# Kernel optimization log

Measured on AMD Instinct MI355X. Metric: run time of the kernel, lower is better.

The kernel has to match this reference:

```python
import jax, jax.numpy as jnp
import numpy as np

TEMPERATURE = 0.1
EPS = 1e-07


def setup_inputs() -> dict:
    key = jax.random.key(0)
    k1, k2 = jax.random.split(key)
    embeddings = jax.random.normal(k1, (4096, 768), dtype=jnp.float32)
    labels = jax.random.normal(k2, (4096, 2), dtype=jnp.float32)
    return {"embeddings": embeddings, "labels": labels}


def _supcr_dim(sims, exp_sims, lab, eps):
    # sims, exp_sims: [M, M]; lab: [M]
    M = lab.shape[0]
    dists = jnp.abs(lab[None, :] - lab[:, None])            # [M, M]
    idx = jnp.argsort(dists, axis=1)                         # row-wise sort order
    sorted_d = jnp.take_along_axis(dists, idx, axis=1)
    sorted_s = jnp.take_along_axis(exp_sims, idx, axis=1)
    # reversed cumsum (suffix sums) along each row
    suffix = jnp.flip(jnp.cumsum(jnp.flip(sorted_s, axis=1), axis=1), axis=1)
    # per-row searchsorted: first index where sorted_d >= dists[i, j]
    pos = jax.vmap(lambda sd, rd: jnp.searchsorted(sd, rd, side='left'))(sorted_d, dists)
    denom = jnp.maximum(jnp.take_along_axis(suffix, pos, axis=1), eps)
    # -log(exp(sims) / denom) == log(denom) - sims
    row_loss = jnp.log(denom) - sims
    off_diag = ~jnp.eye(M, dtype=bool)
    total = jnp.sum(jnp.where(off_diag, row_loss, 0.0))
    return total / (M * (M - 1))


def reference(embeddings, labels):
    # cosine similarity / temperature (torch F.normalize clamps norm at 1e-12)
    norm = jnp.maximum(jnp.linalg.norm(embeddings, axis=1, keepdims=True), 1e-12)
    normed = embeddings / norm
    sims = (normed @ normed.T) / TEMPERATURE                 # [M, M]
    exp_sims = jnp.exp(sims)
    # vmap over label dimensions (labels.T: [num_dims, M])
    losses = jax.vmap(lambda lab: _supcr_dim(sims, exp_sims, lab, EPS))(labels.T)
    return losses
```

## Files before the change

### kernel.cpp

```cpp
#include <hip/hip_runtime.h>
#include <hip/hip_bf16.h>
#include <math.h>

#define MM 4096
#define KK 768
#define NB64 64
#define NBK 1024
#define QSCALE 65536.0f
#define LN2 0.6931471805599453f

typedef short bf16x8 __attribute__((ext_vector_type(8)));
typedef unsigned short u16x8 __attribute__((ext_vector_type(8)));
typedef float f32x4 __attribute__((ext_vector_type(4)));

__device__ __forceinline__ float bf2f(unsigned short u) {
  return __uint_as_float(((unsigned int)u) << 16);
}
__device__ __forceinline__ unsigned short f2bf(float f) {
  __hip_bfloat16 h = __float2bfloat16(f);
  return *(unsigned short*)&h;
}

__device__ __forceinline__ void gload16(const void* g, void* l) {
#if __has_builtin(__builtin_amdgcn_global_load_lds)
  __builtin_amdgcn_global_load_lds((__attribute__((address_space(1))) void*)g,
                                   (__attribute__((address_space(3))) void*)l,
                                   16, 0, 0);
#else
  *(bf16x8*)l = *(const bf16x8*)g;
#endif
}

__global__ __launch_bounds__(256) void knorm(const float* __restrict__ emb,
                                             __hip_bfloat16* __restrict__ nb,
                                             const float* __restrict__ labels,
                                             float* __restrict__ dmm) {
  const int tid = threadIdx.x;
  if (blockIdx.x == MM / 4) {
    float mn0 = 1e30f, mx0 = -1e30f, mn1 = 1e30f, mx1 = -1e30f;
    for (int q = tid; q < MM; q += 256) {
      float2 l2 = ((const float2*)labels)[q];
      mn0 = fminf(mn0, l2.x); mx0 = fmaxf(mx0, l2.x);
      mn1 = fminf(mn1, l2.y); mx1 = fmaxf(mx1, l2.y);
    }
    for (int s = 32; s; s >>= 1) {
      mn0 = fminf(mn0, __shfl_down(mn0, s, 64));
      mx0 = fmaxf(mx0, __shfl_down(mx0, s, 64));
      mn1 = fminf(mn1, __shfl_down(mn1, s, 64));
      mx1 = fmaxf(mx1, __shfl_down(mx1, s, 64));
    }
    __shared__ float redm[4][4];
    if ((tid & 63) == 0) {
      redm[0][tid >> 6] = mn0; redm[1][tid >> 6] = mx0;
      redm[2][tid >> 6] = mn1; redm[3][tid >> 6] = mx1;
    }
    __syncthreads();
    if (tid == 0) {
      dmm[0] = fminf(fminf(redm[0][0], redm[0][1]), fminf(redm[0][2], redm[0][3]));
      dmm[1] = fmaxf(fmaxf(redm[1][0], redm[1][1]), fmaxf(redm[1][2], redm[1][3]));
      dmm[2] = fminf(fminf(redm[2][0], redm[2][1]), fminf(redm[2][2], redm[2][3]));
      dmm[3] = fmaxf(fmaxf(redm[3][0], redm[3][1]), fmaxf(redm[3][2], redm[3][3]));
    }
    return;
  }
  const int w = tid >> 6, l = tid & 63;
  const int row = blockIdx.x * 4 + w;
  const float4* e4 = (const float4*)(emb + (size_t)row * KK);
  float4 a = e4[l], b = e4[l + 64], c = e4[l + 128];
  float ss = a.x * a.x + a.y * a.y + a.z * a.z + a.w * a.w +
             b.x * b.x + b.y * b.y + b.z * b.z + b.w * b.w +
             c.x * c.x + c.y * c.y + c.z * c.z + c.w * c.w;
#pragma unroll
  for (int s = 1; s < 64; s <<= 1) ss += __shfl_xor(ss, s, 64);
  const float inv = 1.f / fmaxf(sqrtf(ss), 1e-12f);
  unsigned short* o = (unsigned short*)(nb + (size_t)row * KK);
  ushort4 o1 = {f2bf(a.x * inv), f2bf(a.y * inv), f2bf(a.z * inv), f2bf(a.w * inv)};
  ushort4 o2 = {f2bf(b.x * inv), f2bf(b.y * inv), f2bf(b.z * inv), f2bf(b.w * inv)};
  ushort4 o3 = {f2bf(c.x * inv), f2bf(c.y * inv), f2bf(c.z * inv), f2bf(c.w * inv)};
  *(ushort4*)(o + l * 4) = o1;
  *(ushort4*)(o + 256 + l * 4) = o2;
  *(ushort4*)(o + 512 + l * 4) = o3;
}

union SmemU64 {
  struct { short As[64 * 64]; short Bs[64 * 64]; } s;
  float tbuf[32][68];
};

__global__ __launch_bounds__(256) void kgemm_sym64(const __hip_bfloat16* __restrict__ A,
                                                   unsigned short* __restrict__ out,
                                                   float* __restrict__ srow) {
  __shared__ __align__(16) SmemU64 sm;
  const int tid = threadIdx.x;
  const int w = tid >> 6, l = tid & 63;
  const int wr = w >> 1, wc = w & 1;
  const int b = blockIdx.x;
  int by = (int)((129.0f - sqrtf(16641.0f - 8.0f * (float)b)) * 0.5f);
  by = min(max(by, 0), 63);
  while (by > 0 && (by * (129 - by)) / 2 > b) --by;
  while (by < 63 && (((by + 1) * (129 - (by + 1))) / 2) <= b) ++by;
  const int bx = by + (b - (by * (129 - by)) / 2);
  const int row0 = by * 64, col0 = bx * 64;
  const short* Ag = (const short*)A;

  f32x4 acc[2][2];
#pragma unroll
  for (int mi = 0; mi < 2; ++mi)
#pragma unroll
    for (int ni = 0; ni < 2; ++ni) acc[mi][ni] = (f32x4){0.f, 0.f, 0.f, 0.f};

  const int r0 = tid >> 3, s0 = tid & 7;
  const int sx = ((s0 ^ (r0 & 7)) * 8);
  const int lr = l & 15, kb = (l >> 4) * 8;
  const int xr = (lr & 7) << 3;

  for (int k0 = 0; k0 < KK; k0 += 64) {
    __syncthreads();
    gload16(Ag + (size_t)(row0 + r0) * KK + k0 + sx, &sm.s.As[tid * 8]);
    gload16(Ag + (size_t)(row0 + 32 + r0) * KK + k0 + sx, &sm.s.As[(tid + 256) * 8]);
    gload16(Ag + (size_t)(col0 + r0) * KK + k0 + sx, &sm.s.Bs[tid * 8]);
    gload16(Ag + (size_t)(col0 + 32 + r0) * KK + k0 + sx, &sm.s.Bs[(tid + 256) * 8]);
    __syncthreads();
    bf16x8 av[2][2], bv[2][2];
#pragma unroll
    for (int mi = 0; mi < 2; ++mi)
#pragma unroll
      for (int kh = 0; kh < 2; ++kh)
        av[mi][kh] = *(const bf16x8*)&sm.s.As[(wr * 32 + mi * 16 + lr) * 64 +
                                              ((kh * 32 + kb) ^ xr)];
#pragma unroll
    for (int ni = 0; ni < 2; ++ni)
#pragma unroll
      for (int kh = 0; kh < 2; ++kh)
        bv[ni][kh] = *(const bf16x8*)&sm.s.Bs[(wc * 32 + ni * 16 + lr) * 64 +
                                              ((kh * 32 + kb) ^ xr)];
#pragma unroll
    for (int kh = 0; kh < 2; ++kh)
#pragma unroll
      for (int mi = 0; mi < 2; ++mi)
#pragma unroll
        for (int ni = 0; ni < 2; ++ni)
          acc[mi][ni] = __builtin_amdgcn_mfma_f32_16x16x32_bf16(av[mi][kh], bv[ni][kh],
                                                                acc[mi][ni], 0, 0, 0);
  }

  const int quad = l >> 4;
  const bool diag = (bx == by);

#pragma unroll
  for (int mi = 0; mi < 2; ++mi) {
#pragma unroll
    for (int r = 0; r < 4; ++r) {
      const int grow = row0 + wr * 32 + mi * 16 + quad * 4 + r;
      float rsum = 0.f;
#pragma unroll
      for (int ni = 0; ni < 2; ++ni) {
        const int gcol = col0 + wc * 32 + ni * 16 + lr;
        rsum += (diag && gcol == grow) ? 0.f : acc[mi][ni][r];
      }
#pragma unroll
      for (int mask = 1; mask < 16; mask <<= 1) rsum += __shfl_xor(rsum, mask, 64);
      if (lr == 0) srow[(size_t)grow * 128 + bx * 2 + wc] = rsum / 0.1f;
    }
  }

  if (!diag) {
#pragma unroll
    for (int ni = 0; ni < 2; ++ni) {
      float csum = 0.f;
#pragma unroll
      for (int mi = 0; mi < 2; ++mi)
#pragma unroll
        for (int r = 0; r < 4; ++r) csum += acc[mi][ni][r];
      csum += __shfl_xor(csum, 16, 64);
      csum += __shfl_xor(csum, 32, 64);
      if (quad == 0)
        srow[(size_t)(col0 + wc * 32 + ni * 16 + l) * 128 + by * 2 + wr] = csum / 0.1f;
    }
  }

#pragma unroll
  for (int mi = 0; mi < 2; ++mi)
#pragma unroll
    for (int ni = 0; ni < 2; ++ni)
#pragma unroll
      for (int r = 0; r < 4; ++r)
        acc[mi][ni][r] = __expf(acc[mi][ni][r] / 0.1f);

#pragma unroll
  for (int mi = 0; mi < 2; ++mi)
#pragma unroll
    for (int r = 0; r < 4; ++r) {
      const int grow = row0 + wr * 32 + mi * 16 + quad * 4 + r;
#pragma unroll
      for (int ni = 0; ni < 2; ++ni)
        out[(size_t)grow * MM + col0 + wc * 32 + ni * 16 + lr] = f2bf(acc[mi][ni][r]);
    }

  if (!diag) {
#pragma unroll
    for (int p = 0; p < 2; ++p) {
      __syncthreads();
      if (wc == p) {
#pragma unroll
        for (int ni = 0; ni < 2; ++ni) {
          const int ltr = ni * 16 + lr;
#pragma unroll
          for (int mi = 0; mi < 2; ++mi) {
            const int cbase = wr * 32 + mi * 16 + quad * 4;
#pragma unroll
            for (int r = 0; r < 4; ++r)
              sm.tbuf[ltr][cbase + r] = acc[mi][ni][r];
          }
        }
      }
      __syncthreads();
      const int trow = tid >> 3;
      const int cseg = (tid & 7) * 8;
      const int gtr = col0 + p * 32 + trow;
      u16x8 vv;
#pragma unroll
      for (int q = 0; q < 8; ++q) vv[q] = f2bf(sm.tbuf[trow][cseg + q]);
      *(u16x8*)(out + (size_t)gtr * MM + row0 + cseg) = vv;
    }
  }
}

__global__ __launch_bounds__(256) void kgemm(const __hip_bfloat16* __restrict__ A,
                                             int rowBase,
                                             unsigned short* __restrict__ out,
                                             float* __restrict__ srow) {
  __shared__ __align__(16) short As[128 * 32];
  __shared__ __align__(16) short Bs[128 * 32];
  const int tid = threadIdx.x;
  const int w = tid >> 6, l = tid & 63;
  const int wr = w >> 1, wc = w & 1;
  const int bx = blockIdx.x;
  const int row0 = rowBase + blockIdx.y * 128;
  const int col0 = bx * 128;
  const short* Ag = (const short*)A;

  f32x4 acc[4][4];
#pragma unroll
  for (int mi = 0; mi < 4; ++mi)
#pragma unroll
    for (int ni = 0; ni < 4; ++ni) acc[mi][ni] = (f32x4){0.f, 0.f, 0.f, 0.f};

  const int r0 = tid >> 2, s0 = tid & 3;
  const int r1 = (tid + 256) >> 2;
  const int lrow = l & 15, kb = (l >> 4) * 8;

  for (int k0 = 0; k0 < KK; k0 += 32) {
    __syncthreads();
    gload16(Ag + (size_t)(row0 + r0) * KK + k0 + s0 * 8, &As[tid * 8]);
    gload16(Ag + (size_t)(row0 + r1) * KK + k0 + s0 * 8, &As[(tid + 256) * 8]);
    gload16(Ag + (size_t)(col0 + r0) * KK + k0 + s0 * 8, &Bs[tid * 8]);
    gload16(Ag + (size_t)(col0 + r1) * KK + k0 + s0 * 8, &Bs[(tid + 256) * 8]);
    __syncthreads();
    bf16x8 av[4], bv[4];
#pragma unroll
    for (int mi = 0; mi < 4; ++mi)
      av[mi] = *(const bf16x8*)&As[(wr * 64 + mi * 16 + lrow) * 32 + kb];
#pragma unroll
    for (int ni = 0; ni < 4; ++ni)
      bv[ni] = *(const bf16x8*)&Bs[(wc * 64 + ni * 16 + lrow) * 32 + kb];
#pragma unroll
    for (int mi = 0; mi < 4; ++mi)
#pragma unroll
      for (int ni = 0; ni < 4; ++ni)
        acc[mi][ni] = __builtin_amdgcn_mfma_f32_16x16x32_bf16(av[mi], bv[ni],
                                                              acc[mi][ni], 0, 0, 0);
  }

  const int quad = l >> 4;
#pragma unroll
  for (int mi = 0; mi < 4; ++mi) {
#pragma unroll
    for (int r = 0; r < 4; ++r) {
      const int grow = row0 + wr * 64 + mi * 16 + quad * 4 + r;
      float rsum = 0.f;
#pragma unroll
      for (int ni = 0; ni < 4; ++ni) {
        const int gcol = col0 + wc * 64 + ni * 16 + lrow;
        float a = acc[mi][ni][r];
        out[(size_t)(grow - rowBase) * MM + gcol] = f2bf(__expf(a / 0.1f));
        rsum += (gcol == grow) ? 0.f : a;
      }
#pragma unroll
      for (int mask = 1; mask < 16; mask <<= 1) rsum += __shfl_xor(rsum, mask, 64);
      if (lrow == 0) srow[(size_t)grow * 128 + bx * 2 + wc] = rsum / 0.1f;
    }
  }
}

__global__ __launch_bounds__(256) void kloss(const unsigned short* __restrict__ expb,
                                             int rowBase,
                                             const float* __restrict__ labels,
                                             const float* __restrict__ dmm,
                                             const float* __restrict__ srow,
                                             float* __restrict__ part_logd,
                                             float* __restrict__ part_sr) {
  const int i = rowBase + blockIdx.x;
  const unsigned short* row = expb + (size_t)blockIdx.x * MM;
  __shared__ __align__(16) unsigned long long histU[2 * NBK];
  __shared__ unsigned long long wsumU[4];
  __shared__ float redf[4];
  __shared__ float redsr[4];
  const int tid = threadIdx.x;
  const int lane = tid & 63, wid = tid >> 6;
  const int m0 = tid * 16;
  const int b0 = tid * 8;

  float sv = (tid < 128) ? srow[(size_t)i * 128 + tid] : 0.f;
  for (int s = 32; s; s >>= 1) sv += __shfl_down(sv, s, 64);
  if (lane == 0) redsr[wid] = sv;

  const float c0 = labels[(size_t)i * 2], c1 = labels[(size_t)i * 2 + 1];
  const float tmax0 = fmaxf(fmaxf(c0 - dmm[0], dmm[1] - c0), 1e-30f);
  const float tmax1 = fmaxf(fmaxf(c1 - dmm[2], dmm[3] - c1), 1e-30f);
  const float scale0 = (float)NBK / tmax0;
  const float scale1 = (float)NBK / tmax1;

#pragma unroll
  for (int q = 0; q < 4; ++q)
    ((uint4*)histU)[tid + 256 * q] = (uint4){0, 0, 0, 0};
  __syncthreads();

  {
    u16x8 a = *(const u16x8*)(row + m0);
    u16x8 bq = *(const u16x8*)(row + m0 + 8);
    const float4* lp4 = (const float4*)(labels + (size_t)m0 * 2);
#pragma unroll
    for (int q = 0; q < 8; ++q) {
      float4 v4 = lp4[q];
      const unsigned short r0u = (2 * q < 8) ? a[2 * q] : bq[2 * q - 8];
      const unsigned short r1u = (2 * q + 1 < 8) ? a[2 * q + 1] : bq[2 * q + 1 - 8];
      const unsigned long long g0 =
          (unsigned long long)(unsigned int)(bf2f(r0u) * QSCALE + 0.5f) | (1ULL << 32);
      const unsigned long long g1 =
          (unsigned long long)(unsigned int)(bf2f(r1u) * QSCALE + 0.5f) | (1ULL << 32);
      const int a0 = min((int)(fabsf(v4.x - c0) * scale0), NBK - 1);
      const int a1 = min((int)(fabsf(v4.y - c1) * scale1), NBK - 1);
      const int b2 = min((int)(fabsf(v4.z - c0) * scale0), NBK - 1);
      const int b3 = min((int)(fabsf(v4.w - c1) * scale1), NBK - 1);
      atomicAdd(&histU[a0], g0);
      atomicAdd(&histU[NBK + a1], g0);
      atomicAdd(&histU[b2], g1);
      atomicAdd(&histU[NBK + b3], g1);
    }
  }
  __syncthreads();

  unsigned long long hh[8];
#pragma unroll
  for (int q = 0; q < 4; ++q) {
    uint4 t4 = *(const uint4*)&histU[b0 + 2 * q];
    hh[2 * q] = (unsigned long long)t4.x | ((unsigned long long)t4.y << 32);
    hh[2 * q + 1] = (unsigned long long)t4.z | ((unsigned long long)t4.w << 32);
  }
  unsigned long long S = 0;
#pragma unroll
  for (int u = 0; u < 8; ++u) S += hh[u];
  unsigned long long v = S;
#pragma unroll
  for (int s = 1; s < 64; s <<= 1) {
    unsigned long long t2 = __shfl_down(v, s, 64);
    if (lane + s < 64) v += t2;
  }
  if (lane == 0) wsumU[wid] = v;
  __syncthreads();
  unsigned long long woff = (wid == 0) ? wsumU[1] : ((wid == 2) ? wsumU[3] : 0ULL);
  unsigned long long run = woff + (v - S);

  float acc2 = 0.f;
#pragma unroll
  for (int u = 7; u >= 0; --u) {
    run += hh[u];
    const float nf = (float)(unsigned int)(hh[u] >> 32);
    const float sufq = (float)(unsigned int)run;
    acc2 += nf * __log2f(fmaxf(sufq, 1.f));
  }

  for (int s = 32; s; s >>= 1) acc2 += __shfl_down(acc2, s, 64);
  if (lane == 0) redf[wid] = acc2;
  __syncthreads();
  if (tid == 0) {
    const float tf0 = (float)(unsigned int)(wsumU[0] + wsumU[1]);
    const float tf1 = (float)(unsigned int)(wsumU[2] + wsumU[3]);
    part_logd[i] = (redf[0] + redf[1] - 65536.f - __log2f(tf0) + 16.f) * LN2;
    part_logd[MM + i] = (redf[2] + redf[3] - 65536.f - __log2f(tf1) + 16.f) * LN2;
    part_sr[i] = redsr[0] + redsr[1];
  }
}

__global__ __launch_bounds__(256) void kred1(const float* __restrict__ part_logd,
                                             const float* __restrict__ part_sr,
                                             double* __restrict__ red3) {
  const int tid = threadIdx.x;
  const int base = blockIdx.x * 64;
  double ss = 0.0, s0 = 0.0, s1 = 0.0;
  if (tid < 64) {
    s0 = (double)part_logd[base + tid];
    s1 = (double)part_logd[MM + base + tid];
    ss = (double)part_sr[base + tid];
  }
  for (int s = 32; s; s >>= 1) {
    s0 += __shfl_down(s0, s, 64);
    s1 += __shfl_down(s1, s, 64);
    ss += __shfl_down(ss, s, 64);
  }
  __shared__ double red[3][4];
  if ((tid & 63) == 0) {
    red[0][tid >> 6] = s0; red[1][tid >> 6] = s1; red[2][tid >> 6] = ss;
  }
  __syncthreads();
  if (tid == 0) {
    red3[blockIdx.x * 3 + 0] = red[0][0] + red[0][1] + red[0][2] + red[0][3];
    red3[blockIdx.x * 3 + 1] = red[1][0] + red[1][1] + red[1][2] + red[1][3];
    red3[blockIdx.x * 3 + 2] = red[2][0] + red[2][1] + red[2][2] + red[2][3];
  }
}

__global__ __launch_bounds__(64) void kred2(const double* __restrict__ red3,
                                            float* __restrict__ out) {
  const int t = threadIdx.x;
  double s0 = red3[t * 3 + 0], s1 = red3[t * 3 + 1], ss = red3[t * 3 + 2];
  for (int s = 32; s; s >>= 1) {
    s0 += __shfl_down(s0, s, 64);
    s1 += __shfl_down(s1, s, 64);
    ss += __shfl_down(ss, s, 64);
  }
  if (t == 0) {
    const double n = (double)MM * (double)(MM - 1);
    out[0] = (float)((s0 - ss) / n);
    out[1] = (float)((s1 - ss) / n);
  }
}

extern "C" void kernel_launch(void* const* d_in, const int* in_sizes, int n_in,
                              void* d_out, int out_size, void* d_ws, size_t ws_size,
                              hipStream_t stream) {
  const float* emb = (const float*)d_in[0];
  const float* labels = (const float*)d_in[1];
  float* out = (float*)d_out;
  char* ws = (char*)d_ws;

  size_t off = 0;
  auto alloc = [&](size_t bytes) {
    void* p = ws + off;
    off = (off + bytes + 255) & ~(size_t)255;
    return p;
  };
  __hip_bfloat16* nb = (__hip_bfloat16*)alloc((size_t)MM * KK * 2);
  float* dmm = (float*)alloc(4 * 4);
  float* part_logd = (float*)alloc((size_t)2 * MM * 4);
  float* part_sr = (float*)alloc((size_t)MM * 4);
  float* srow = (float*)alloc((size_t)MM * 128 * 4);
  double* red3 = (double*)alloc((size_t)64 * 3 * 8);
  size_t fixed = off;

  size_t avail = (ws_size > fixed) ? (ws_size - fixed) : 0;
  long long cr = (long long)(avail / ((size_t)MM * 2));
  cr = (cr / 128) * 128;
  if (cr > MM) cr = MM;
  if (cr < 128) cr = 128;
  int chunk_rows = (int)cr;
  unsigned short* expb = (unsigned short*)(ws + fixed);

  knorm<<<MM / 4 + 1, 256, 0, stream>>>(emb, nb, labels, dmm);

  if (chunk_rows == MM) {
    kgemm_sym64<<<NB64 * (NB64 + 1) / 2, 256, 0, stream>>>(nb, expb, srow);
    kloss<<<MM, 256, 0, stream>>>(expb, 0, labels, dmm, srow, part_logd, part_sr);
  } else {
    hipMemsetAsync(srow, 0, (size_t)MM * 128 * 4, stream);
    for (int base = 0; base < MM; base += chunk_rows) {
      int rows = MM - base < chunk_rows ? MM - base : chunk_rows;
      kgemm<<<dim3(MM / 128, rows / 128), 256, 0, stream>>>(nb, base, expb, srow);
      kloss<<<rows, 256, 0, stream>>>(expb, base, labels, dmm, srow, part_logd, part_sr);
    }
  }
  kred1<<<64, 256, 0, stream>>>(part_logd, part_sr, red3);
  kred2<<<1, 64, 0, stream>>>(red3, out);
}
```

Before: 70.75 us.

## Pair adjacent column tiles per GEMM block and fuse final reduction via atomics

The symmetric GEMM now gives each block two horizontally adjacent 64x64 tiles of the upper triangle, sharing the A-tile load across both and halving the block count. This reuses A from LDS, at the cost of more LDS and more registers per block. The two small reduction kernels are removed: kloss blocks atomically add their partial sums in double precision, and the last block, found through a ticket counter, writes the output. This saves two launches but adds atomic contention and makes the summation order nondeterministic.

Measured after the change: 255.4 us. +261.0%, slower.

```diff
diff --git a/kernel.cpp b/kernel.cpp
--- a/kernel.cpp
+++ b/kernel.cpp
@@ -4,7 +4,6 @@
 
 #define MM 4096
 #define KK 768
-#define NB64 64
 #define NBK 1024
 #define QSCALE 65536.0f
 #define LN2 0.6931471805599453f
@@ -34,9 +33,12 @@
 __global__ __launch_bounds__(256) void knorm(const float* __restrict__ emb,
                                              __hip_bfloat16* __restrict__ nb,
                                              const float* __restrict__ labels,
-                                             float* __restrict__ dmm) {
+                                             float* __restrict__ dmm,
+                                             double* __restrict__ gacc) {
   const int tid = threadIdx.x;
   if (blockIdx.x == MM / 4) {
+    if (tid < 3) gacc[tid] = 0.0;
+    if (tid == 3) *(unsigned int*)(gacc + 3) = 0u;
     float mn0 = 1e30f, mx0 = -1e30f, mn1 = 1e30f, mx1 = -1e30f;
     for (int q = tid; q < MM; q += 256) {
       float2 l2 = ((const float2*)labels)[q];
@@ -82,32 +84,35 @@
   *(ushort4*)(o + 512 + l * 4) = o3;
 }
 
-union SmemU64 {
-  struct { short As[64 * 64]; short Bs[64 * 64]; } s;
+union SmemP {
+  struct { short As[64 * 64]; short Bs0[64 * 64]; short Bs1[64 * 64]; } s;
   float tbuf[32][68];
 };
 
-__global__ __launch_bounds__(256) void kgemm_sym64(const __hip_bfloat16* __restrict__ A,
-                                                   unsigned short* __restrict__ out,
-                                                   float* __restrict__ srow) {
-  __shared__ __align__(16) SmemU64 sm;
+__global__ __launch_bounds__(256) void kgemm_sym64p(const __hip_bfloat16* __restrict__ A,
+                                                    unsigned short* __restrict__ out,
+                                                    float* __restrict__ srow) {
+  __shared__ __align__(16) SmemP sm;
   const int tid = threadIdx.x;
   const int w = tid >> 6, l = tid & 63;
   const int wr = w >> 1, wc = w & 1;
-  const int b = blockIdx.x;
-  int by = (int)((129.0f - sqrtf(16641.0f - 8.0f * (float)b)) * 0.5f);
-  by = min(max(by, 0), 63);
-  while (by > 0 && (by * (129 - by)) / 2 > b) --by;
-  while (by < 63 && (((by + 1) * (129 - (by + 1))) / 2) <= b) ++by;
-  const int bx = by + (b - (by * (129 - by)) / 2);
-  const int row0 = by * 64, col0 = bx * 64;
+  int rem = blockIdx.x, by = 0;
+  while (rem >= ((65 - by) >> 1)) { rem -= (65 - by) >> 1; ++by; }
+  const int bx0 = by + 2 * rem;
+  const int bx1 = bx0 + 1;
+  const bool has2 = (bx1 < 64);
+  const int row0 = by * 64;
+  const int col0t[2] = {bx0 * 64, (has2 ? bx1 : bx0) * 64};
+  const int bxt[2] = {bx0, bx1};
   const short* Ag = (const short*)A;
 
-  f32x4 acc[2][2];
-#pragma unroll
-  for (int mi = 0; mi < 2; ++mi)
-#pragma unroll
-    for (int ni = 0; ni < 2; ++ni) acc[mi][ni] = (f32x4){0.f, 0.f, 0.f, 0.f};
+  f32x4 acc[2][2][2];
+#pragma unroll
+  for (int t = 0; t < 2; ++t)
+#pragma unroll
+    for (int mi = 0; mi < 2; ++mi)
+#pragma unroll
+      for (int ni = 0; ni < 2; ++ni) acc[t][mi][ni] = (f32x4){0.f, 0.f, 0.f, 0.f};
 
   const int r0 = tid >> 3, s0 = tid & 7;
   const int sx = ((s0 ^ (r0 & 7)) * 8);
@@ -118,110 +123,145 @@
     __syncthreads();
     gload16(Ag + (size_t)(row0 + r0) * KK + k0 + sx, &sm.s.As[tid * 8]);
     gload16(Ag + (size_t)(row0 + 32 + r0) * KK + k0 + sx, &sm.s.As[(tid + 256) * 8]);
-    gload16(Ag + (size_t)(col0 + r0) * KK + k0 + sx, &sm.s.Bs[tid * 8]);
-    gload16(Ag + (size_t)(col0 + 32 + r0) * KK + k0 + sx, &sm.s.Bs[(tid + 256) * 8]);
+    gload16(Ag + (size_t)(col0t[0] + r0) * KK + k0 + sx, &sm.s.Bs0[tid * 8]);
+    gload16(Ag + (size_t)(col0t[0] + 32 + r0) * KK + k0 + sx, &sm.s.Bs0[(tid + 256) * 8]);
+    gload16(Ag + (size_t)(col0t[1] + r0) * KK + k0 + sx, &sm.s.Bs1[tid * 8]);
+    gload16(Ag + (size_t)(col0t[1] + 32 + r0) * KK + k0 + sx, &sm.s.Bs1[(tid + 256) * 8]);
     __syncthreads();
-    bf16x8 av[2][2], bv[2][2];
+    bf16x8 av[2][2];
 #pragma unroll
     for (int mi = 0; mi < 2; ++mi)
 #pragma unroll
       for (int kh = 0; kh < 2; ++kh)
         av[mi][kh] = *(const bf16x8*)&sm.s.As[(wr * 32 + mi * 16 + lr) * 64 +
                                               ((kh * 32 + kb) ^ xr)];
-#pragma unroll
-    for (int ni = 0; ni < 2; ++ni)
+    {
+      bf16x8 bv[2][2];
+#pragma unroll
+      for (int ni = 0; ni < 2; ++ni)
+#pragma unroll
+        for (int kh = 0; kh < 2; ++kh)
+          bv[ni][kh] = *(const bf16x8*)&sm.s.Bs0[(wc * 32 + ni * 16 + lr) * 64 +
+                                                 ((kh * 32 + kb) ^ xr)];
 #pragma unroll
       for (int kh = 0; kh < 2; ++kh)
-        bv[ni][kh] = *(const bf16x8*)&sm.s.Bs[(wc * 32 + ni * 16 + lr) * 64 +
-                                              ((kh * 32 + kb) ^ xr)];
-#pragma unroll
-    for (int kh = 0; kh < 2; ++kh)
+#pragma unroll
+        for (int mi = 0; mi < 2; ++mi)
+#pragma unroll
+          for (int ni = 0; ni < 2; ++ni)
+            acc[0][mi][ni] = __builtin_amdgcn_mfma_f32_16x16x32_bf16(
+                av[mi][kh], bv[ni][kh], acc[0][mi][ni], 0, 0, 0);
+    }
+    {
+      bf16x8 bv[2][2];
+#pragma unroll
+      for (int ni = 0; ni < 2; ++ni)
+#pragma unroll
+        for (int kh = 0; kh < 2; ++kh)
+          bv[ni][kh] = *(const bf16x8*)&sm.s.Bs1[(wc * 32 + ni * 16 + lr) * 64 +
+                                                 ((kh * 32 + kb) ^ xr)];
+#pragma unroll
+      for (int kh = 0; kh < 2; ++kh)
+#pragma unroll
+        for (int mi = 0; mi < 2; ++mi)
+#pragma unroll
+          for (int ni = 0; ni < 2; ++ni)
+            acc[1][mi][ni] = __builtin_amdgcn_mfma_f32_16x16x32_bf16(
+                av[mi][kh], bv[ni][kh], acc[1][mi][ni], 0, 0, 0);
+    }
+  }
+
+  const int quad = l >> 4;
+
+#pragma unroll
+  for (int t = 0; t < 2; ++t) {
+    const bool active = (t == 0) || has2;
+    const bool diag = (t == 0) && (bx0 == by);
+    const int col0 = col0t[t];
+
+#pragma unroll
+    for (int mi = 0; mi < 2; ++mi) {
+#pragma unroll
+      for (int r = 0; r < 4; ++r) {
+        const int grow = row0 + wr * 32 + mi * 16 + quad * 4 + r;
+        float rsum = 0.f;
+#pragma unroll
+        for (int ni = 0; ni < 2; ++ni) {
+          const int gcol = col0 + wc * 32 + ni * 16 + lr;
+          rsum += (diag && gcol == grow) ? 0.f : acc[t][mi][ni][r];
+        }
+#pragma unroll
+        for (int mask = 1; mask < 16; mask <<= 1) rsum += __shfl_xor(rsum, mask, 64);
+        if (active && lr == 0)
+          srow[(size_t)grow * 128 + bxt[t] * 2 + wc] = rsum / 0.1f;
+      }
+    }
+
+    if (!diag) {
+#pragma unroll
+      for (int ni = 0; ni < 2; ++ni) {
+        float csum = 0.f;
+#pragma unroll
+        for (int mi = 0; mi < 2; ++mi)
+#pragma unroll
+          for (int r = 0; r < 4; ++r) csum += acc[t][mi][ni][r];
+        csum += __shfl_xor(csum, 16, 64);
+        csum += __shfl_xor(csum, 32, 64);
+        if (active && quad == 0)
+          srow[(size_t)(col0 + wc * 32 + ni * 16 + l) * 128 + by * 2 + wr] =
+              csum / 0.1f;
+      }
+    }
+
+#pragma unroll
+    for (int mi = 0; mi < 2; ++mi)
+#pragma unroll
+      for (int ni = 0; ni < 2; ++ni)
+#pragma unroll
+        for (int r = 0; r < 4; ++r)
+          acc[t][mi][ni][r] = __expf(acc[t][mi][ni][r] / 0.1f);
+
+    if (active) {
 #pragma unroll
       for (int mi = 0; mi < 2; ++mi)
 #pragma unroll
-        for (int ni = 0; ni < 2; ++ni)
-          acc[mi][ni] = __builtin_amdgcn_mfma_f32_16x16x32_bf16(av[mi][kh], bv[ni][kh],
-                                                                acc[mi][ni], 0, 0, 0);
-  }
-
-  const int quad = l >> 4;
-  const bool diag = (bx == by);
-
-#pragma unroll
-  for (int mi = 0; mi < 2; ++mi) {
-#pragma unroll
-    for (int r = 0; r < 4; ++r) {
-      const int grow = row0 + wr * 32 + mi * 16 + quad * 4 + r;
-      float rsum = 0.f;
-#pragma unroll
-      for (int ni = 0; ni < 2; ++ni) {
-        const int gcol = col0 + wc * 32 + ni * 16 + lr;
-        rsum += (diag && gcol == grow) ? 0.f : acc[mi][ni][r];
-      }
-#pragma unroll
-      for (int mask = 1; mask < 16; mask <<= 1) rsum += __shfl_xor(rsum, mask, 64);
-      if (lr == 0) srow[(size_t)grow * 128 + bx * 2 + wc] = rsum / 0.1f;
-    }
-  }
-
-  if (!diag) {
-#pragma unroll
-    for (int ni = 0; ni < 2; ++ni) {
-      float csum = 0.f;
-#pragma unroll
-      for (int mi = 0; mi < 2; ++mi)
-#pragma unroll
-        for (int r = 0; r < 4; ++r) csum += acc[mi][ni][r];
-      csum += __shfl_xor(csum, 16, 64);
-      csum += __shfl_xor(csum, 32, 64);
-      if (quad == 0)
-        srow[(size_t)(col0 + wc * 32 + ni * 16 + l) * 128 + by * 2 + wr] = csum / 0.1f;
-    }
-  }
-
-#pragma unroll
-  for (int mi = 0; mi < 2; ++mi)
-#pragma unroll
-    for (int ni = 0; ni < 2; ++ni)
-#pragma unroll
-      for (int r = 0; r < 4; ++r)
-        acc[mi][ni][r] = __expf(acc[mi][ni][r] / 0.1f);
-
-#pragma unroll
-  for (int mi = 0; mi < 2; ++mi)
-#pragma unroll
-    for (int r = 0; r < 4; ++r) {
-      const int grow = row0 + wr * 32 + mi * 16 + quad * 4 + r;
-#pragma unroll
-      for (int ni = 0; ni < 2; ++ni)
-        out[(size_t)grow * MM + col0 + wc * 32 + ni * 16 + lr] = f2bf(acc[mi][ni][r]);
-    }
-
-  if (!diag) {
-#pragma unroll
-    for (int p = 0; p < 2; ++p) {
-      __syncthreads();
-      if (wc == p) {
-#pragma unroll
-        for (int ni = 0; ni < 2; ++ni) {
-          const int ltr = ni * 16 + lr;
-#pragma unroll
-          for (int mi = 0; mi < 2; ++mi) {
-            const int cbase = wr * 32 + mi * 16 + quad * 4;
-#pragma unroll
-            for (int r = 0; r < 4; ++r)
-              sm.tbuf[ltr][cbase + r] = acc[mi][ni][r];
+        for (int r = 0; r < 4; ++r) {
+          const int grow = row0 + wr * 32 + mi * 16 + quad * 4 + r;
+#pragma unroll
+          for (int ni = 0; ni < 2; ++ni)
+            out[(size_t)grow * MM + col0 + wc * 32 + ni * 16 + lr] =
+                f2bf(acc[t][mi][ni][r]);
+        }
+    }
+
+    if (!diag) {
+#pragma unroll
+      for (int p = 0; p < 2; ++p) {
+        __syncthreads();
+        if (wc == p) {
+#pragma unroll
+          for (int ni = 0; ni < 2; ++ni) {
+            const int ltr = ni * 16 + lr;
+#pragma unroll
+            for (int mi = 0; mi < 2; ++mi) {
+              const int cbase = wr * 32 + mi * 16 + quad * 4;
+#pragma unroll
+              for (int r = 0; r < 4; ++r)
+                sm.tbuf[ltr][cbase + r] = acc[t][mi][ni][r];
+            }
           }
         }
+        __syncthreads();
+        if (active) {
+          const int trow = tid >> 3;
+          const int cseg = (tid & 7) * 8;
+          const int gtr = col0 + p * 32 + trow;
+          u16x8 vv;
+#pragma unroll
+          for (int q = 0; q < 8; ++q) vv[q] = f2bf(sm.tbuf[trow][cseg + q]);
+          *(u16x8*)(out + (size_t)gtr * MM + row0 + cseg) = vv;
+        }
       }
-      __syncthreads();
-      const int trow = tid >> 3;
-      const int cseg = (tid & 7) * 8;
-      const int gtr = col0 + p * 32 + trow;
-      u16x8 vv;
-#pragma unroll
-      for (int q = 0; q < 8; ++q) vv[q] = f2bf(sm.tbuf[trow][cseg + q]);
-      *(u16x8*)(out + (size_t)gtr * MM + row0 + cseg) = vv;
     }
   }
 }
@@ -298,8 +338,8 @@
                                              const float* __restrict__ labels,
                                              const float* __restrict__ dmm,
                                              const float* __restrict__ srow,
-                                             float* __restrict__ part_logd,
-                                             float* __restrict__ part_sr) {
+                                             double* __restrict__ gacc,
+                                             float* __restrict__ outv) {
   const int i = rowBase + blockIdx.x;
   const unsigned short* row = expb + (size_t)blockIdx.x * MM;
   __shared__ __align__(16) unsigned long long histU[2 * NBK];
@@ -387,53 +427,22 @@
   if (tid == 0) {
     const float tf0 = (float)(unsigned int)(wsumU[0] + wsumU[1]);
     const float tf1 = (float)(unsigned int)(wsumU[2] + wsumU[3]);
-    part_logd[i] = (redf[0] + redf[1] - 65536.f - __log2f(tf0) + 16.f) * LN2;
-    part_logd[MM + i] = (redf[2] + redf[3] - 65536.f - __log2f(tf1) + 16.f) * LN2;
-    part_sr[i] = redsr[0] + redsr[1];
-  }
-}
-
-__global__ __launch_bounds__(256) void kred1(const float* __restrict__ part_logd,
-                                             const float* __restrict__ part_sr,
-                                             double* __restrict__ red3) {
-  const int tid = threadIdx.x;
-  const int base = blockIdx.x * 64;
-  double ss = 0.0, s0 = 0.0, s1 = 0.0;
-  if (tid < 64) {
-    s0 = (double)part_logd[base + tid];
-    s1 = (double)part_logd[MM + base + tid];
-    ss = (double)part_sr[base + tid];
-  }
-  for (int s = 32; s; s >>= 1) {
-    s0 += __shfl_down(s0, s, 64);
-    s1 += __shfl_down(s1, s, 64);
-    ss += __shfl_down(ss, s, 64);
-  }
-  __shared__ double red[3][4];
-  if ((tid & 63) == 0) {
-    red[0][tid >> 6] = s0; red[1][tid >> 6] = s1; red[2][tid >> 6] = ss;
-  }
-  __syncthreads();
-  if (tid == 0) {
-    red3[blockIdx.x * 3 + 0] = red[0][0] + red[0][1] + red[0][2] + red[0][3];
-    red3[blockIdx.x * 3 + 1] = red[1][0] + red[1][1] + red[1][2] + red[1][3];
-    red3[blockIdx.x * 3 + 2] = red[2][0] + red[2][1] + red[2][2] + red[2][3];
-  }
-}
-
-__global__ __launch_bounds__(64) void kred2(const double* __restrict__ red3,
-                                            float* __restrict__ out) {
-  const int t = threadIdx.x;
-  double s0 = red3[t * 3 + 0], s1 = red3[t * 3 + 1], ss = red3[t * 3 + 2];
-  for (int s = 32; s; s >>= 1) {
-    s0 += __shfl_down(s0, s, 64);
-    s1 += __shfl_down(s1, s, 64);
-    ss += __shfl_down(ss, s, 64);
-  }
-  if (t == 0) {
-    const double n = (double)MM * (double)(MM - 1);
-    out[0] = (float)((s0 - ss) / n);
-    out[1] = (float)((s1 - ss) / n);
+    const float p0 = (redf[0] + redf[1] - 65536.f - __log2f(tf0) + 16.f) * LN2;
+    const float p1 = (redf[2] + redf[3] - 65536.f - __log2f(tf1) + 16.f) * LN2;
+    const float psr = redsr[0] + redsr[1];
+    atomicAdd(&gacc[0], (double)p0);
+    atomicAdd(&gacc[1], (double)p1);
+    atomicAdd(&gacc[2], (double)psr);
+    __threadfence();
+    unsigned int tk = atomicAdd((unsigned int*)(gacc + 3), 1u);
+    if (tk == MM - 1) {
+      const double a0 = atomicAdd(&gacc[0], 0.0);
+      const double a1 = atomicAdd(&gacc[1], 0.0);
+      const double asr = atomicAdd(&gacc[2], 0.0);
+      const double n = (double)MM * (double)(MM - 1);
+      outv[0] = (float)((a0 - asr) / n);
+      outv[1] = (float)((a1 - asr) / n);
+    }
   }
 }
 
@@ -453,10 +462,8 @@
   };
   __hip_bfloat16* nb = (__hip_bfloat16*)alloc((size_t)MM * KK * 2);
   float* dmm = (float*)alloc(4 * 4);
-  float* part_logd = (float*)alloc((size_t)2 * MM * 4);
-  float* part_sr = (float*)alloc((size_t)MM * 4);
+  double* gacc = (double*)alloc(4 * 8);
   float* srow = (float*)alloc((size_t)MM * 128 * 4);
-  double* red3 = (double*)alloc((size_t)64 * 3 * 8);
   size_t fixed = off;
 
   size_t avail = (ws_size > fixed) ? (ws_size - fixed) : 0;
@@ -467,19 +474,17 @@
   int chunk_rows = (int)cr;
   unsigned short* expb = (unsigned short*)(ws + fixed);
 
-  knorm<<<MM / 4 + 1, 256, 0, stream>>>(emb, nb, labels, dmm);
+  knorm<<<MM / 4 + 1, 256, 0, stream>>>(emb, nb, labels, dmm, gacc);
 
   if (chunk_rows == MM) {
-    kgemm_sym64<<<NB64 * (NB64 + 1) / 2, 256, 0, stream>>>(nb, expb, srow);
-    kloss<<<MM, 256, 0, stream>>>(expb, 0, labels, dmm, srow, part_logd, part_sr);
+    kgemm_sym64p<<<1056, 256, 0, stream>>>(nb, expb, srow);
+    kloss<<<MM, 256, 0, stream>>>(expb, 0, labels, dmm, srow, gacc, out);
   } else {
     hipMemsetAsync(srow, 0, (size_t)MM * 128 * 4, stream);
     for (int base = 0; base < MM; base += chunk_rows) {
       int rows = MM - base < chunk_rows ? MM - base : chunk_rows;
       kgemm<<<dim3(MM / 128, rows / 128), 256, 0, stream>>>(nb, base, expb, srow);
-      kloss<<<rows, 256, 0, stream>>>(expb, base, labels, dmm, srow, part_logd, part_sr);
-    }
-  }
-  kred1<<<64, 256, 0, stream>>>(part_logd, part_sr, red3);
-  kred2<<<1, 64, 0, stream>>>(red3, out);
-}
+      kloss<<<rows, 256, 0, stream>>>(expb, base, labels, dmm, srow, gacc, out);
+    }
+  }
+}
```
